# Kernel tuning notes

Hardware: AMD Instinct MI355X
Metric: run time of the kernel (lower is better)

## Reference

```python
import jax, jax.numpy as jnp
import numpy as np

BLOCK_SIZE = 64


def _dequant_weight(weight_packed, centroids, scales):
    # weight_packed: [out, in//2] bytes; each byte packs two 4-bit codes.
    # torch.cartesian_prod ordering: byte v -> (centroids[v >> 4], centroids[v & 0xF])
    hi = weight_packed >> 4
    lo = weight_packed & 0xF
    out_f, packed_in = weight_packed.shape
    w = jnp.stack([centroids[hi], centroids[lo]], axis=-1).reshape(out_f, packed_in * 2)
    num_blocks = scales.shape[1]
    w = (w.reshape(out_f, num_blocks, -1) * scales[:, :, None]).reshape(out_f, packed_in * 2)
    return w  # [out, in]


def setup_inputs() -> dict:
    key = jax.random.key(0)
    k1, k2, k3, k4 = jax.random.split(key, 4)
    B, S, IN, OUT = 2, 4096, 4096, 4096
    x = jax.random.normal(k1, (B, S, IN), dtype=jnp.float32)
    weight_packed = jax.random.randint(k2, (OUT, IN // 2), 0, 256, dtype=jnp.int32)
    centroids = jax.random.normal(k3, (16,), dtype=jnp.float32)
    scales = jax.random.uniform(k4, (OUT, IN // BLOCK_SIZE), dtype=jnp.float32)
    return {"x": x, "weight_packed": weight_packed, "centroids": centroids, "scales": scales}


def reference(x, weight_packed, centroids, scales):
    orig_shape = x.shape
    in_features = orig_shape[-1]
    x_flat = x.reshape(-1, in_features)  # [M, in]
    w = _dequant_weight(weight_packed, centroids, scales)  # [out, in]
    out = x_flat @ w.T  # [M, out]
    return out.reshape(*orig_shape[:-1], w.shape[0])
```

## Files before the change

kernel.cpp:

```cpp
#include <hip/hip_runtime.h>
#include <hip/hip_bf16.h>
#include <stdint.h>

typedef __bf16 bf16_t;
typedef bf16_t bf16x8 __attribute__((ext_vector_type(8)));
typedef float f32x4 __attribute__((ext_vector_type(4)));

#define GAS __attribute__((address_space(1)))
#define LAS __attribute__((address_space(3)))

__device__ __forceinline__ void async_load16(void* g, void* l) {
    __builtin_amdgcn_global_load_lds((GAS void*)g, (LAS void*)l, 16, 0, 0);
}

__global__ void cast_f32_to_bf16(const float* __restrict__ x, bf16_t* __restrict__ y, long n8) {
    long t = (long)blockIdx.x * blockDim.x + threadIdx.x;
    if (t >= n8) return;
    const float4* xp = (const float4*)x;
    float4 v0 = xp[2 * t], v1 = xp[2 * t + 1];
    bf16x8 o;
    o[0] = (bf16_t)v0.x; o[1] = (bf16_t)v0.y; o[2] = (bf16_t)v0.z; o[3] = (bf16_t)v0.w;
    o[4] = (bf16_t)v1.x; o[5] = (bf16_t)v1.y; o[6] = (bf16_t)v1.z; o[7] = (bf16_t)v1.w;
    ((bf16x8*)y)[t] = o;
}

__global__ void dequant_w(const int* __restrict__ wp, const float* __restrict__ cen,
                          const float* __restrict__ scl, bf16_t* __restrict__ W, int n4) {
    __shared__ float c[16];
    if (threadIdx.x < 16) c[threadIdx.x] = cen[threadIdx.x];
    __syncthreads();
    int t = blockIdx.x * blockDim.x + threadIdx.x;
    if (t >= n4) return;
    int4 v = ((const int4*)wp)[t];
    int p   = t << 2;
    int o   = p >> 11;
    int pin = p & 2047;
    float s = scl[(o << 6) + (pin >> 5)];
    int vv[4] = {v.x, v.y, v.z, v.w};
    bf16x8 outv;
#pragma unroll
    for (int i = 0; i < 4; ++i) {
        int b = vv[i];
        outv[2 * i]     = (bf16_t)(c[(b >> 4) & 15] * s);
        outv[2 * i + 1] = (bf16_t)(c[b & 15] * s);
    }
    ((bf16x8*)W)[t] = outv;
}

#define BM 128
#define BN 128
#define BK 32

__global__ __launch_bounds__(256, 3) void gemm_bf16_nt(
    const bf16_t* __restrict__ A, const bf16_t* __restrict__ B,
    float* __restrict__ C, int M, int N, int K)
{
    __shared__ bf16_t lA[BM * BK];
    __shared__ bf16_t lB[BN * BK];

    const int tid  = threadIdx.x;
    const int wave = tid >> 6;
    const int lane = tid & 63;
    const int wm   = (wave >> 1) * 64;
    const int wn   = (wave & 1) * 64;

    const long m0 = (long)blockIdx.y * BM;
    const long n0 = (long)blockIdx.x * BN;

    const int c0   = wave * 64 + lane;
    const int c1   = c0 + 256;
    const int row0 = c0 >> 2, kk0 = (c0 & 3) * 8;
    const int row1 = c1 >> 2, kk1 = (c1 & 3) * 8;

    bf16_t* An = (bf16_t*)A;
    bf16_t* Bn = (bf16_t*)B;
    bf16_t* a0 = An + (m0 + row0) * K + kk0;
    bf16_t* a1 = An + (m0 + row1) * K + kk1;
    bf16_t* b0 = Bn + (n0 + row0) * K + kk0;
    bf16_t* b1 = Bn + (n0 + row1) * K + kk1;

    bf16_t* lA0 = lA + (wave * 64) * 8;
    bf16_t* lA1 = lA0 + 256 * 8;
    bf16_t* lB0 = lB + (wave * 64) * 8;
    bf16_t* lB1 = lB0 + 256 * 8;

    const int qm = lane & 15;
    const int qk = (lane >> 4) * 8;
    const bf16_t* pa = lA + (wm + qm) * BK + qk;
    const bf16_t* pb = lB + (wn + qm) * BK + qk;

    f32x4 acc[4][4] = {};

    for (int k0 = 0; k0 < K; k0 += BK) {
        async_load16(a0 + k0, lA0);
        async_load16(a1 + k0, lA1);
        async_load16(b0 + k0, lB0);
        async_load16(b1 + k0, lB1);
        __syncthreads();
        bf16x8 af[4], bfv[4];
#pragma unroll
        for (int i = 0; i < 4; ++i) af[i] = *(const bf16x8*)(pa + i * 16 * BK);
#pragma unroll
        for (int j = 0; j < 4; ++j) bfv[j] = *(const bf16x8*)(pb + j * 16 * BK);
#pragma unroll
        for (int i = 0; i < 4; ++i)
#pragma unroll
            for (int j = 0; j < 4; ++j)
                acc[i][j] = __builtin_amdgcn_mfma_f32_16x16x32_bf16(af[i], bfv[j], acc[i][j], 0, 0, 0);
        __syncthreads();
    }

    const int crow = (lane >> 4) * 4;
    const int ccol = lane & 15;
#pragma unroll
    for (int i = 0; i < 4; ++i)
#pragma unroll
        for (int r = 0; r < 4; ++r) {
            float* cp = C + (m0 + wm + i * 16 + crow + r) * N + (n0 + wn + ccol);
#pragma unroll
            for (int j = 0; j < 4; ++j)
                cp[j * 16] = acc[i][j][r];
        }
}

__global__ void fallback_qgemm(const float* __restrict__ x, const int* __restrict__ wp,
                               const float* __restrict__ cen, const float* __restrict__ scl,
                               float* __restrict__ out, int M, int N, int Kp) {
    __shared__ float c[16];
    if (threadIdx.x < 16) c[threadIdx.x] = cen[threadIdx.x];
    __syncthreads();
    int n = blockIdx.x * blockDim.x + threadIdx.x;
    int m = blockIdx.y;
    if (n >= N) return;
    const float* xr = x + (long)m * (Kp * 2);
    const int*   wr = wp + (long)n * Kp;
    int nb = Kp / 32;
    float acc = 0.f;
    for (int b = 0; b < nb; ++b) {
        float s  = scl[n * nb + b];
        float pa = 0.f;
        for (int j = 0; j < 32; ++j) {
            int v = wr[b * 32 + j];
            pa += xr[(b * 32 + j) * 2]     * c[(v >> 4) & 15]
                + xr[(b * 32 + j) * 2 + 1] * c[v & 15];
        }
        acc += s * pa;
    }
    out[(long)m * N + n] = acc;
}

extern "C" void kernel_launch(void* const* d_in, const int* in_sizes, int n_in,
                              void* d_out, int out_size, void* d_ws, size_t ws_size,
                              hipStream_t stream) {
    const float* x   = (const float*)d_in[0];
    const int*   wp  = (const int*)d_in[1];
    const float* cen = (const float*)d_in[2];
    const float* scl = (const float*)d_in[3];
    float* out = (float*)d_out;

    const int  IN  = 4096;
    const int  OUT = 4096;
    const long M   = (long)in_sizes[0] / IN;

    size_t need = (size_t)(M * IN + (long)OUT * IN) * sizeof(bf16_t);
    if (ws_size >= need) {
        bf16_t* xb = (bf16_t*)d_ws;
        bf16_t* Wb = xb + M * IN;
        long n8 = M * IN / 8;
        cast_f32_to_bf16<<<dim3((unsigned)((n8 + 255) / 256)), dim3(256), 0, stream>>>(x, xb, n8);
        int n4 = OUT * (IN / 2) / 4;
        dequant_w<<<dim3((n4 + 255) / 256), dim3(256), 0, stream>>>(wp, cen, scl, Wb, n4);
        dim3 grid(OUT / BN, (unsigned)(M / BM));
        gemm_bf16_nt<<<grid, dim3(256), 0, stream>>>(xb, Wb, out, (int)M, OUT, IN);
    } else {
        dim3 grid(OUT / 256, (unsigned)M);
        fallback_qgemm<<<grid, dim3(256), 0, stream>>>(x, wp, cen, scl, out, (int)M, OUT, IN / 2);
    }
}
```

Baseline: 533.9 us.

## Fuse cast and dequant into one prep kernel; XOR-swizzle GEMM LDS layout

Merges the activation cast and weight dequant into a single launch that branches on block index, and narrows the cast to one float4 per thread. In the GEMM, the k-chunk each thread loads into LDS is XOR-swizzled by row bits, and the fragment reads use the matching swizzle, to reduce LDS bank conflicts on the bf16x8 reads. This saves a kernel launch and should make the MFMA operand loads more efficient. The risk is a swizzle mismatch between writer and reader, and a more divergent prep kernel.

```diff
diff --git a/kernel.cpp b/kernel.cpp
--- a/kernel.cpp
+++ b/kernel.cpp
@@ -3,6 +3,7 @@
 #include <stdint.h>
 
 typedef __bf16 bf16_t;
+typedef bf16_t bf16x4 __attribute__((ext_vector_type(4)));
 typedef bf16_t bf16x8 __attribute__((ext_vector_type(8)));
 typedef float f32x4 __attribute__((ext_vector_type(4)));
 
@@ -13,38 +14,36 @@
     __builtin_amdgcn_global_load_lds((GAS void*)g, (LAS void*)l, 16, 0, 0);
 }
 
-__global__ void cast_f32_to_bf16(const float* __restrict__ x, bf16_t* __restrict__ y, long n8) {
-    long t = (long)blockIdx.x * blockDim.x + threadIdx.x;
-    if (t >= n8) return;
-    const float4* xp = (const float4*)x;
-    float4 v0 = xp[2 * t], v1 = xp[2 * t + 1];
-    bf16x8 o;
-    o[0] = (bf16_t)v0.x; o[1] = (bf16_t)v0.y; o[2] = (bf16_t)v0.z; o[3] = (bf16_t)v0.w;
-    o[4] = (bf16_t)v1.x; o[5] = (bf16_t)v1.y; o[6] = (bf16_t)v1.z; o[7] = (bf16_t)v1.w;
-    ((bf16x8*)y)[t] = o;
-}
-
-__global__ void dequant_w(const int* __restrict__ wp, const float* __restrict__ cen,
-                          const float* __restrict__ scl, bf16_t* __restrict__ W, int n4) {
-    __shared__ float c[16];
-    if (threadIdx.x < 16) c[threadIdx.x] = cen[threadIdx.x];
-    __syncthreads();
-    int t = blockIdx.x * blockDim.x + threadIdx.x;
-    if (t >= n4) return;
-    int4 v = ((const int4*)wp)[t];
-    int p   = t << 2;
-    int o   = p >> 11;
-    int pin = p & 2047;
-    float s = scl[(o << 6) + (pin >> 5)];
-    int vv[4] = {v.x, v.y, v.z, v.w};
-    bf16x8 outv;
+__global__ void prep_kernel(const float* __restrict__ x, bf16_t* __restrict__ xb,
+                            const int* __restrict__ wp, const float* __restrict__ cen,
+                            const float* __restrict__ scl, bf16_t* __restrict__ W,
+                            int castBlocks) {
+    if ((int)blockIdx.x < castBlocks) {
+        long t = (long)blockIdx.x * blockDim.x + threadIdx.x;
+        float4 v = ((const float4*)x)[t];
+        bf16x4 o;
+        o[0] = (bf16_t)v.x; o[1] = (bf16_t)v.y; o[2] = (bf16_t)v.z; o[3] = (bf16_t)v.w;
+        ((bf16x4*)xb)[t] = o;
+    } else {
+        __shared__ float c[16];
+        if (threadIdx.x < 16) c[threadIdx.x] = cen[threadIdx.x];
+        __syncthreads();
+        int t = ((int)blockIdx.x - castBlocks) * blockDim.x + threadIdx.x;
+        int4 v = ((const int4*)wp)[t];
+        int p   = t << 2;
+        int o   = p >> 11;
+        int pin = p & 2047;
+        float s = scl[(o << 6) + (pin >> 5)];
+        int vv[4] = {v.x, v.y, v.z, v.w};
+        bf16x8 outv;
 #pragma unroll
-    for (int i = 0; i < 4; ++i) {
-        int b = vv[i];
-        outv[2 * i]     = (bf16_t)(c[(b >> 4) & 15] * s);
-        outv[2 * i + 1] = (bf16_t)(c[b & 15] * s);
+        for (int i = 0; i < 4; ++i) {
+            int b = vv[i];
+            outv[2 * i]     = (bf16_t)(c[(b >> 4) & 15] * s);
+            outv[2 * i + 1] = (bf16_t)(c[b & 15] * s);
+        }
+        ((bf16x8*)W)[t] = outv;
     }
-    ((bf16x8*)W)[t] = outv;
 }
 
 #define BM 128
@@ -67,10 +66,10 @@
     const long m0 = (long)blockIdx.y * BM;
     const long n0 = (long)blockIdx.x * BN;
 
-    const int c0   = wave * 64 + lane;
-    const int c1   = c0 + 256;
-    const int row0 = c0 >> 2, kk0 = (c0 & 3) * 8;
-    const int row1 = c1 >> 2, kk1 = (c1 & 3) * 8;
+    const int s0   = wave * 64 + lane;
+    const int s1   = s0 + 256;
+    const int row0 = s0 >> 2, kk0 = ((s0 & 3) ^ ((s0 >> 3) & 3)) * 8;
+    const int row1 = s1 >> 2, kk1 = ((s1 & 3) ^ ((s1 >> 3) & 3)) * 8;
 
     bf16_t* An = (bf16_t*)A;
     bf16_t* Bn = (bf16_t*)B;
@@ -85,9 +84,11 @@
     bf16_t* lB1 = lB0 + 256 * 8;
 
     const int qm = lane & 15;
-    const int qk = (lane >> 4) * 8;
-    const bf16_t* pa = lA + (wm + qm) * BK + qk;
-    const bf16_t* pb = lB + (wn + qm) * BK + qk;
+    const int kc = lane >> 4;
+    const int sw = (qm >> 1) & 3;
+    const int kks = (kc ^ sw) * 8;
+    const bf16_t* pa = lA + (wm + qm) * BK + kks;
+    const bf16_t* pb = lB + (wn + qm) * BK + kks;
 
     f32x4 acc[4][4] = {};
 
@@ -166,10 +167,10 @@
     if (ws_size >= need) {
         bf16_t* xb = (bf16_t*)d_ws;
         bf16_t* Wb = xb + M * IN;
-        long n8 = M * IN / 8;
-        cast_f32_to_bf16<<<dim3((unsigned)((n8 + 255) / 256)), dim3(256), 0, stream>>>(x, xb, n8);
-        int n4 = OUT * (IN / 2) / 4;
-        dequant_w<<<dim3((n4 + 255) / 256), dim3(256), 0, stream>>>(wp, cen, scl, Wb, n4);
+        int castBlocks = (int)(M * IN / 4 / 256);
+        int deqBlocks  = OUT * (IN / 2) / 4 / 256;
+        prep_kernel<<<dim3(castBlocks + deqBlocks), dim3(256), 0, stream>>>(
+            x, xb, wp, cen, scl, Wb, castBlocks);
         dim3 grid(OUT / BN, (unsigned)(M / BM));
         gemm_bf16_nt<<<grid, dim3(256), 0, stream>>>(xb, Wb, out, (int)M, OUT, IN);
     } else {
```

Result: no change. 529.1 us (-0.9%).
